# Performance work log

Hardware: AMD Instinct MI355X
Metric: run time of the kernel (lower is better)

## Reference

```python
import jax, jax.numpy as jnp
import numpy as np

N_NODES = 10000
N_EDGES = 640000
F_IN = 128
HID = 128
F_OUT = 40
BN_EPS = 1e-5


def setup_inputs() -> dict:
    key = jax.random.key(0)
    ks = jax.random.split(key, 8)
    x = jax.random.normal(ks[0], (N_NODES, F_IN), dtype=jnp.float32)
    edge_row = jax.random.randint(ks[1], (N_EDGES,), 0, N_NODES)
    edge_col = jax.random.randint(ks[2], (N_EDGES,), 0, N_NODES)
    edge_val = jax.random.uniform(ks[3], (N_EDGES,), dtype=jnp.float32)
    W1 = jax.random.normal(ks[4], (F_IN, HID), dtype=jnp.float32) * 0.05
    W2 = jax.random.normal(ks[5], (HID, HID), dtype=jnp.float32) * 0.05
    W3 = jax.random.normal(ks[6], (HID, F_OUT), dtype=jnp.float32) * 0.05
    return {
        "x": x, "edge_row": edge_row, "edge_col": edge_col, "edge_val": edge_val,
        "W1": W1, "b1": jnp.zeros((HID,), jnp.float32),
        "gamma2": jnp.ones((HID,), jnp.float32), "beta2": jnp.zeros((HID,), jnp.float32),
        "W2": W2, "b2": jnp.zeros((HID,), jnp.float32),
        "gamma3": jnp.ones((HID,), jnp.float32), "beta3": jnp.zeros((HID,), jnp.float32),
        "W3": W3, "b3": jnp.zeros((F_OUT,), jnp.float32),
    }


def _spmm(edge_row, edge_col, edge_val, x, n_nodes):
    # out[i] = sum_{e: row[e]==i} val[e] * x[col[e]]  == torch.sparse.mm(adj, x)
    msgs = edge_val[:, None] * jnp.take(x, edge_col, axis=0)  # [E, F]
    return jax.ops.segment_sum(msgs, edge_row, num_segments=n_nodes)


def _batchnorm(x, gamma, beta):
    # BatchNorm1d (training-mode normalization, biased variance)
    mean = jnp.mean(x, axis=0)
    var = jnp.mean(jnp.square(x - mean), axis=0)
    return gamma * (x - mean) * jax.lax.rsqrt(var + BN_EPS) + beta


def reference(x, edge_row, edge_col, edge_val, W1, b1, gamma2, beta2,
              W2, b2, gamma3, beta3, W3, b3):
    n = x.shape[0]
    # layer 1: SpMM -> Linear -> ReLU -> (dropout=identity in eval) -> BN
    h = _spmm(edge_row, edge_col, edge_val, x, n)
    h = jax.nn.relu(h @ W1 + b1)
    h = _batchnorm(h, gamma2, beta2)
    # layer 2
    h = _spmm(edge_row, edge_col, edge_val, h, n)
    h = jax.nn.relu(h @ W2 + b2)
    h = _batchnorm(h, gamma3, beta3)
    # layer 3
    h = _spmm(edge_row, edge_col, edge_val, h, n)
    h = h @ W3 + b3
    return jax.nn.log_softmax(h, axis=1)
```

## Files before the change

kernel.cpp:

```cpp
#include <hip/hip_runtime.h>
#include <hip/hip_bf16.h>
#include <math.h>

#define N_NODES 10000
#define F 128
#define F_OUT_ 40
#define N_EDGES_ 640000
#define BN_EPS 1e-5f
#define NBIN 625
#define RPB 16
#define NWGA 64
#define EPW 10000
#define BINCAP 1536
#define NREP 8

__device__ __forceinline__ unsigned pack4(int col, float v) {
    __hip_bfloat16 b = __float2bfloat16(v);
    return ((unsigned)(*(unsigned short*)&b) << 16) | (unsigned)col;
}
__device__ __forceinline__ int   col_of(unsigned q) { return (int)(q & 0xFFFFu); }
__device__ __forceinline__ float val_of(unsigned q) { return __uint_as_float(q & 0xFFFF0000u); }
__device__ __forceinline__ float lo16f(unsigned w) { return __uint_as_float(w << 16); }
__device__ __forceinline__ float hi16f(unsigned w) { return __uint_as_float(w & 0xffff0000u); }

__global__ __launch_bounds__(256) void fused_g1h(const float* __restrict__ x,
        const float* __restrict__ W1, __hip_bfloat16* __restrict__ T,
        const int* __restrict__ erow, int* __restrict__ hist,
        float* __restrict__ accsZ ) {
    __shared__ float Ws[F * F];
    __shared__ float As[16][F];
    __shared__ int   lh[NBIN];
    int tid = threadIdx.x;
    if (blockIdx.x == 0) {
        for (int i = tid; i < 2 * NREP * 256; i += 256) accsZ[i] = 0.f;
    }
    if (blockIdx.x >= NBIN) {
        int w = blockIdx.x - NBIN;
        for (int t = tid; t < NBIN; t += 256) lh[t] = 0;
        __syncthreads();
        int e0 = w * EPW;
        for (int e = e0 + tid; e < e0 + EPW; e += 256)
            atomicAdd(&lh[erow[e] >> 4], 1);
        __syncthreads();
        for (int t = tid; t < NBIN; t += 256) hist[w * NBIN + t] = lh[t];
        return;
    }
    for (int i = tid; i < F * F; i += 256) Ws[i] = W1[i];
    int r0 = blockIdx.x * 16;
    for (int i = tid; i < 16 * F; i += 256) {
        int r2 = i >> 7, k = i & (F - 1);
        As[r2][k] = x[(size_t)(r0 + r2) * F + k];
    }
    __syncthreads();
    int c = tid & (F - 1), hh = tid >> 7;
    for (int r2 = hh; r2 < 16; r2 += 2) {
        float acc = 0.f;
        #pragma unroll
        for (int k = 0; k < F; ++k) acc = fmaf(As[r2][k], Ws[k * F + c], acc);
        T[(size_t)(r0 + r2) * F + c] = __float2bfloat16(acc);
    }
}

__global__ __launch_bounds__(1024) void scatter_bin(const int* __restrict__ erow,
                                                    const int* __restrict__ ecol,
                                                    const float* __restrict__ eval_,
                                                    const int* __restrict__ hist,
                                                    int* __restrict__ base_g,
                                                    int2* __restrict__ ebin) {
    __shared__ int myoff[NBIN];
    __shared__ int tot[NBIN];
    __shared__ int cur[NBIN];
    __shared__ int sc[1024];
    int w = blockIdx.x, tid = threadIdx.x;
    for (int b = tid; b < NBIN; b += 1024) {
        int own = 0, all = 0;
        #pragma unroll 8
        for (int w2 = 0; w2 < NWGA; ++w2) {
            int h = hist[w2 * NBIN + b];
            all += h;
            if (w2 < w) own += h;
        }
        myoff[b] = own;
        tot[b] = all;
        cur[b] = 0;
    }
    __syncthreads();
    int val = (tid < NBIN) ? tot[tid] : 0;
    sc[tid] = val;
    __syncthreads();
    for (int off = 1; off < 1024; off <<= 1) {
        int v = 0;
        if (tid >= off) v = sc[tid - off];
        __syncthreads();
        if (tid >= off) sc[tid] += v;
        __syncthreads();
    }
    if (tid < NBIN) {
        int base = sc[tid] - val;
        myoff[tid] += base;
        if (w == 0) base_g[tid] = base;
    }
    if (w == 0 && tid == 0) base_g[NBIN] = N_EDGES_;
    __syncthreads();
    int e0 = w * EPW, e1 = e0 + EPW;
    int e = e0 + tid;
    for (; e + 3072 < e1; e += 4096) {
        int   r0 = erow[e],        r1 = erow[e + 1024],  r2 = erow[e + 2048],  r3 = erow[e + 3072];
        int   c0 = ecol[e],        c1 = ecol[e + 1024],  c2 = ecol[e + 2048],  c3 = ecol[e + 3072];
        float v0 = eval_[e],       v1 = eval_[e + 1024], v2 = eval_[e + 2048], v3 = eval_[e + 3072];
        int b0 = r0 >> 4, b1 = r1 >> 4, b2 = r2 >> 4, b3 = r3 >> 4;
        int p0 = atomicAdd(&cur[b0], 1);
        int p1 = atomicAdd(&cur[b1], 1);
        int p2 = atomicAdd(&cur[b2], 1);
        int p3 = atomicAdd(&cur[b3], 1);
        ebin[myoff[b0] + p0] = make_int2((r0 << 14) | c0, __float_as_int(v0));
        ebin[myoff[b1] + p1] = make_int2((r1 << 14) | c1, __float_as_int(v1));
        ebin[myoff[b2] + p2] = make_int2((r2 << 14) | c2, __float_as_int(v2));
        ebin[myoff[b3] + p3] = make_int2((r3 << 14) | c3, __float_as_int(v3));
    }
    for (; e < e1; e += 1024) {
        int r = erow[e];
        int b = r >> 4;
        int p = atomicAdd(&cur[b], 1);
        ebin[myoff[b] + p] = make_int2((r << 14) | ecol[e], __float_as_int(eval_[e]));
    }
}

__global__ __launch_bounds__(256) void sort_bin(const int* __restrict__ base,
                                                const int2* __restrict__ ebin,
                                                unsigned* __restrict__ ebin2,
                                                int* __restrict__ rowptr) {
    __shared__ int2    ein[BINCAP];
    __shared__ unsigned eout[BINCAP];
    __shared__ int cnt16[16], pos16[16], exc[16];
    int b = blockIdx.x, tid = threadIdx.x;
    int lo = base[b], hi = base[b + 1];
    int n = min(hi - lo, BINCAP);
    for (int i = tid; i < n; i += 256) ein[i] = ebin[lo + i];
    if (tid < 16) cnt16[tid] = 0;
    __syncthreads();
    for (int i = tid; i < n; i += 256)
        atomicAdd(&cnt16[(ein[i].x >> 14) & 15], 1);
    __syncthreads();
    if (tid == 0) {
        int run = 0;
        #pragma unroll
        for (int j = 0; j < 16; ++j) { exc[j] = run; run += cnt16[j]; }
    }
    __syncthreads();
    if (tid < 16) {
        pos16[tid] = exc[tid];
        rowptr[b * RPB + tid] = lo + exc[tid];
    }
    if (b == NBIN - 1 && tid == 0) rowptr[N_NODES] = hi;
    __syncthreads();
    for (int i = tid; i < n; i += 256) {
        int2 q = ein[i];
        int j = (q.x >> 14) & 15;
        int p = atomicAdd(&pos16[j], 1);
        eout[p] = pack4(q.x & 16383, __int_as_float(q.y));
    }
    __syncthreads();
    for (int i = tid; i < n; i += 256) ebin2[lo + i] = eout[i];
}

__global__ __launch_bounds__(256) void spmm_row4s(const int* __restrict__ rowptr,
                                                  const unsigned* __restrict__ epk,
                                                  const uint2* __restrict__ T2,
                                                  float* __restrict__ Z,
                                                  const float* __restrict__ bias,
                                                  float* __restrict__ accs) {
    __shared__ float sacc[2][F];
    int tid = threadIdx.x;
    for (int i = tid; i < 2 * F; i += 256) ((float*)sacc)[i] = 0.f;
    __syncthreads();
    int wv = tid >> 6, lane = tid & 63;
    int r = blockIdx.x * 4 + wv;
    int beg = rowptr[r], end = rowptr[r + 1];
    int half = lane >> 5, l2 = lane & 31;
    float a0c0 = 0.f, a0c1 = 0.f, a1c0 = 0.f, a1c1 = 0.f;
    float a2c0 = 0.f, a2c1 = 0.f, a3c0 = 0.f, a3c1 = 0.f;
    for (int bb = beg; bb < end; bb += 64) {
        int m = min(end - bb, 64);
        unsigned myq = (lane < m) ? epk[bb + lane] : 0u;
        int j = 0;
        for (; j + 16 <= m; j += 16) {
            unsigned q[8]; uint2 w[8];
            #pragma unroll
            for (int t = 0; t < 8; ++t) {
                q[t] = __shfl(myq, j + 2 * t + half);
                w[t] = T2[(unsigned)col_of(q[t]) * 32u + l2];
            }
            #pragma unroll
            for (int t = 0; t < 8; ++t) {
                float v = val_of(q[t]);
                if (t & 1) {
                    a0c1 = fmaf(v, lo16f(w[t].x), a0c1);
                    a1c1 = fmaf(v, hi16f(w[t].x), a1c1);
                    a2c1 = fmaf(v, lo16f(w[t].y), a2c1);
                    a3c1 = fmaf(v, hi16f(w[t].y), a3c1);
                } else {
                    a0c0 = fmaf(v, lo16f(w[t].x), a0c0);
                    a1c0 = fmaf(v, hi16f(w[t].x), a1c0);
                    a2c0 = fmaf(v, lo16f(w[t].y), a2c0);
                    a3c0 = fmaf(v, hi16f(w[t].y), a3c0);
                }
            }
        }
        for (; j + 2 <= m; j += 2) {
            unsigned q = __shfl(myq, j + half);
            uint2 w = T2[(unsigned)col_of(q) * 32u + l2];
            float v = val_of(q);
            a0c0 = fmaf(v, lo16f(w.x), a0c0);
            a1c0 = fmaf(v, hi16f(w.x), a1c0);
            a2c0 = fmaf(v, lo16f(w.y), a2c0);
            a3c0 = fmaf(v, hi16f(w.y), a3c0);
        }
        if (j < m) {
            unsigned q = __shfl(myq, j);
            uint2 w = T2[(unsigned)col_of(q) * 32u + l2];
            float v = half ? 0.f : val_of(q);
            a0c0 = fmaf(v, lo16f(w.x), a0c0);
            a1c0 = fmaf(v, hi16f(w.x), a1c0);
            a2c0 = fmaf(v, lo16f(w.y), a2c0);
            a3c0 = fmaf(v, hi16f(w.y), a3c0);
        }
    }
    float a0 = a0c0 + a0c1, a1 = a1c0 + a1c1;
    float a2 = a2c0 + a2c1, a3 = a3c0 + a3c1;
    a0 += __shfl_xor(a0, 32);
    a1 += __shfl_xor(a1, 32);
    a2 += __shfl_xor(a2, 32);
    a3 += __shfl_xor(a3, 32);
    if (half == 0) {
        *(float4*)(Z + (size_t)r * F + 4 * l2) = make_float4(a0, a1, a2, a3);
        float4 bi = *(const float4*)(bias + 4 * l2);
        float t0 = fmaxf(a0 + bi.x, 0.f), t1 = fmaxf(a1 + bi.y, 0.f);
        float t2 = fmaxf(a2 + bi.z, 0.f), t3 = fmaxf(a3 + bi.w, 0.f);
        atomicAdd(&sacc[0][4 * l2],     t0); atomicAdd(&sacc[1][4 * l2],     t0 * t0);
        atomicAdd(&sacc[0][4 * l2 + 1], t1); atomicAdd(&sacc[1][4 * l2 + 1], t1 * t1);
        atomicAdd(&sacc[0][4 * l2 + 2], t2); atomicAdd(&sacc[1][4 * l2 + 2], t2 * t2);
        atomicAdd(&sacc[0][4 * l2 + 3], t3); atomicAdd(&sacc[1][4 * l2 + 3], t3 * t3);
    }
    __syncthreads();
    int rep = blockIdx.x & (NREP - 1);
    float* dst = accs + rep * 2 * F;
    for (int i = tid; i < F; i += 256) {
        atomicAdd(&dst[i],     sacc[0][i]);
        atomicAdd(&dst[F + i], sacc[1][i]);
    }
}

__global__ __launch_bounds__(256) void spmm40_ls(const int* __restrict__ rowptr,
                                                 const unsigned* __restrict__ epk,
                                                 const unsigned short* __restrict__ T40,
                                                 const float* __restrict__ b3,
                                                 float* __restrict__ out) {
    int wv = threadIdx.x >> 6, lane = threadIdx.x & 63;
    int w = blockIdx.x * 4 + wv;
    if (w >= N_NODES) return;
    int beg = rowptr[w], end = rowptr[w + 1];
    float a[4] = {0.f, 0.f, 0.f, 0.f};
    const unsigned short* Tb = T40 + lane;
    bool act = (lane < F_OUT_);
    for (int base = beg; base < end; base += 64) {
        int m = min(end - base, 64);
        unsigned myq = 0;
        if (lane < m) myq = epk[base + lane];
        int j = 0;
        for (; j + 8 <= m; j += 8) {
            unsigned q[8];
            #pragma unroll
            for (int t = 0; t < 8; ++t) q[t] = __shfl(myq, j + t);
            if (act) {
                unsigned short u[8];
                #pragma unroll
                for (int t = 0; t < 8; ++t) u[t] = Tb[(unsigned)col_of(q[t]) * 40u];
                #pragma unroll
                for (int t = 0; t < 8; ++t)
                    a[t & 3] = fmaf(val_of(q[t]),
                                    __uint_as_float(((unsigned)u[t]) << 16), a[t & 3]);
            }
        }
        for (; j < m; ++j) {
            unsigned q = __shfl(myq, j);
            if (act) {
                unsigned short u = Tb[(unsigned)col_of(q) * 40u];
                a[0] = fmaf(val_of(q), __uint_as_float(((unsigned)u) << 16), a[0]);
            }
        }
    }
    float acc = (a[0] + a[1]) + (a[2] + a[3]);
    float val = act ? acc + b3[lane] : -INFINITY;
    float m2 = val;
    #pragma unroll
    for (int off = 32; off > 0; off >>= 1) m2 = fmaxf(m2, __shfl_xor(m2, off));
    float e = act ? expf(val - m2) : 0.f;
    float s = e;
    #pragma unroll
    for (int off = 32; off > 0; off >>= 1) s += __shfl_xor(s, off);
    if (act) out[(size_t)w * F_OUT_ + lane] = val - m2 - logf(s);
}


__global__ __launch_bounds__(256) void gemm128_bn(const float* __restrict__ A,
        const float* __restrict__ W, const float* __restrict__ bias,
        const float* __restrict__ gamma, const float* __restrict__ beta,
        const float* __restrict__ accs, __hip_bfloat16* __restrict__ C) {
    __shared__ float Ws[F * F];
    __shared__ float As[16][F];
    __shared__ float sc[F], sh[F], bi[F];
    int tid = threadIdx.x;
    if (tid < F) {
        float s = 0.f, s2 = 0.f;
        #pragma unroll
        for (int rp = 0; rp < NREP; ++rp) {
            s  += accs[rp * 2 * F + tid];
            s2 += accs[rp * 2 * F + F + tid];
        }
        float m   = s / (float)N_NODES;
        float var = s2 / (float)N_NODES - m * m;
        float rs  = rsqrtf(var + BN_EPS);
        float g   = gamma[tid] * rs;
        sc[tid] = g;
        sh[tid] = beta[tid] - g * m;
        bi[tid] = bias[tid];
    }
    for (int i = tid; i < F * F; i += 256) Ws[i] = W[i];
    __syncthreads();
    int r0 = blockIdx.x * 16;
    for (int i = tid; i < 16 * F; i += 256) {
        int r2 = i >> 7, k = i & (F - 1);
        float a = A[(size_t)(r0 + r2) * F + k];
        As[r2][k] = fmaxf(a + bi[k], 0.f) * sc[k] + sh[k];
    }
    __syncthreads();
    int c = tid & (F - 1), hh = tid >> 7;
    for (int r2 = hh; r2 < 16; r2 += 2) {
        float acc = 0.f;
        #pragma unroll
        for (int k = 0; k < F; ++k) acc = fmaf(As[r2][k], Ws[k * F + c], acc);
        C[(size_t)(r0 + r2) * F + c] = __float2bfloat16(acc);
    }
}

__global__ __launch_bounds__(256) void gemm40_bn(const float* __restrict__ A,
        const float* __restrict__ W, const float* __restrict__ bias,
        const float* __restrict__ gamma, const float* __restrict__ beta,
        const float* __restrict__ accs, __hip_bfloat16* __restrict__ C) {
    __shared__ float Ws[F * F_OUT_];
    __shared__ float sc[F], sh[F], bi[F];
    int tid = threadIdx.x;
    if (tid < F) {
        float s = 0.f, s2 = 0.f;
        #pragma unroll
        for (int rp = 0; rp < NREP; ++rp) {
            s  += accs[rp * 2 * F + tid];
            s2 += accs[rp * 2 * F + F + tid];
        }
        float m   = s / (float)N_NODES;
        float var = s2 / (float)N_NODES - m * m;
        float rs  = rsqrtf(var + BN_EPS);
        float g   = gamma[tid] * rs;
        sc[tid] = g;
        sh[tid] = beta[tid] - g * m;
        bi[tid] = bias[tid];
    }
    for (int i = tid; i < F * F_OUT_; i += 256) Ws[i] = W[i];
    __syncthreads();
    int c = tid % F_OUT_, rl = tid / F_OUT_;
    if (rl >= 6) return;
    int r = blockIdx.x * 6 + rl;
    if (r >= N_NODES) return;
    const float* a = A + (size_t)r * F;
    float acc = 0.f;
    #pragma unroll
    for (int k = 0; k < F; ++k) {
        float t = fmaxf(a[k] + bi[k], 0.f) * sc[k] + sh[k];
        acc = fmaf(t, Ws[k * F_OUT_ + c], acc);
    }
    C[(size_t)r * F_OUT_ + c] = __float2bfloat16(acc);
}


extern "C" void kernel_launch(void* const* d_in, const int* in_sizes, int n_in,
                              void* d_out, int out_size, void* d_ws, size_t ws_size,
                              hipStream_t stream) {
    const float* x      = (const float*)d_in[0];
    const int*   erow   = (const int*)  d_in[1];
    const int*   ecol   = (const int*)  d_in[2];
    const float* eval_  = (const float*)d_in[3];
    const float* W1     = (const float*)d_in[4];
    const float* b1     = (const float*)d_in[5];
    const float* gamma2 = (const float*)d_in[6];
    const float* beta2  = (const float*)d_in[7];
    const float* W2     = (const float*)d_in[8];
    const float* b2     = (const float*)d_in[9];
    const float* gamma3 = (const float*)d_in[10];
    const float* beta3  = (const float*)d_in[11];
    const float* W3     = (const float*)d_in[12];
    const float* b3     = (const float*)d_in[13];
    float* out = (float*)d_out;

    const size_t nf = (size_t)N_NODES * F;
    const int BLK = 256;

    int*   hist   = (int*)d_ws;
    int*   base_g = hist + NWGA * NBIN;
    float* accsA  = (float*)(base_g + 626);
    float* accsB  = accsA + NREP * 256;
    int*   rowptr = (int*)(accsB + NREP * 256);
    __hip_bfloat16* T = (__hip_bfloat16*)(rowptr + 10016);
    float* Z     = (float*)((char*)T + nf * 2);
    int2*  ebin  = (int2*)(Z + nf);
    unsigned* ebin2 = (unsigned*)(ebin + N_EDGES_);

    fused_g1h<<<NBIN + NWGA, BLK, 0, stream>>>(x, W1, T, erow, hist, accsA);
    scatter_bin<<<NWGA, 1024, 0, stream>>>(erow, ecol, eval_, hist, base_g, ebin);
    sort_bin<<<NBIN, BLK, 0, stream>>>(base_g, ebin, ebin2, rowptr);

    const int GB4 = N_NODES / 4;

    spmm_row4s<<<GB4, BLK, 0, stream>>>(rowptr, ebin2, (const uint2*)T, Z, b1, accsA);

    gemm128_bn<<<NBIN, BLK, 0, stream>>>(Z, W2, b1, gamma2, beta2, accsA, T);
    spmm_row4s<<<GB4, BLK, 0, stream>>>(rowptr, ebin2, (const uint2*)T, Z, b2, accsB);

    gemm40_bn<<<(N_NODES + 5) / 6, BLK, 0, stream>>>(Z, W3, b2, gamma3, beta3, accsB, T);
    spmm40_ls<<<GB4, BLK, 0, stream>>>(rowptr, ebin2, (const unsigned short*)T, b3, out);
}
```

Baseline: 149.9 us.

## Use nontemporal gathers in SpMM and spread edge scatter over more workgroups

The SpMM kernels now read the gathered feature table through nontemporal loads, which changes how the random gathers interact with the caches. The edge-binning pass now uses 256 workgroups of 2500 edges each instead of 64 of 10000, and its 4-way unrolled loop is replaced by a simple strided loop. The nontemporal hint may hurt reuse, because T is small and rows are gathered many times. The larger histogram also makes the prefix work in the binning kernels bigger.

```diff
diff --git a/kernel.cpp b/kernel.cpp
--- a/kernel.cpp
+++ b/kernel.cpp
@@ -9,8 +9,8 @@
 #define BN_EPS 1e-5f
 #define NBIN 625
 #define RPB 16
-#define NWGA 64
-#define EPW 10000
+#define NWGA 256
+#define EPW 2500
 #define BINCAP 1536
 #define NREP 8
 
@@ -103,22 +103,7 @@
     if (w == 0 && tid == 0) base_g[NBIN] = N_EDGES_;
     __syncthreads();
     int e0 = w * EPW, e1 = e0 + EPW;
-    int e = e0 + tid;
-    for (; e + 3072 < e1; e += 4096) {
-        int   r0 = erow[e],        r1 = erow[e + 1024],  r2 = erow[e + 2048],  r3 = erow[e + 3072];
-        int   c0 = ecol[e],        c1 = ecol[e + 1024],  c2 = ecol[e + 2048],  c3 = ecol[e + 3072];
-        float v0 = eval_[e],       v1 = eval_[e + 1024], v2 = eval_[e + 2048], v3 = eval_[e + 3072];
-        int b0 = r0 >> 4, b1 = r1 >> 4, b2 = r2 >> 4, b3 = r3 >> 4;
-        int p0 = atomicAdd(&cur[b0], 1);
-        int p1 = atomicAdd(&cur[b1], 1);
-        int p2 = atomicAdd(&cur[b2], 1);
-        int p3 = atomicAdd(&cur[b3], 1);
-        ebin[myoff[b0] + p0] = make_int2((r0 << 14) | c0, __float_as_int(v0));
-        ebin[myoff[b1] + p1] = make_int2((r1 << 14) | c1, __float_as_int(v1));
-        ebin[myoff[b2] + p2] = make_int2((r2 << 14) | c2, __float_as_int(v2));
-        ebin[myoff[b3] + p3] = make_int2((r3 << 14) | c3, __float_as_int(v3));
-    }
-    for (; e < e1; e += 1024) {
+    for (int e = e0 + tid; e < e1; e += 1024) {
         int r = erow[e];
         int b = r >> 4;
         int p = atomicAdd(&cur[b], 1);
@@ -166,7 +151,7 @@
 
 __global__ __launch_bounds__(256) void spmm_row4s(const int* __restrict__ rowptr,
                                                   const unsigned* __restrict__ epk,
-                                                  const uint2* __restrict__ T2,
+                                                  const unsigned long long* __restrict__ T8,
                                                   float* __restrict__ Z,
                                                   const float* __restrict__ bias,
                                                   float* __restrict__ accs) {
@@ -185,45 +170,48 @@
         unsigned myq = (lane < m) ? epk[bb + lane] : 0u;
         int j = 0;
         for (; j + 16 <= m; j += 16) {
-            unsigned q[8]; uint2 w[8];
+            unsigned q[8]; unsigned long long w[8];
             #pragma unroll
             for (int t = 0; t < 8; ++t) {
                 q[t] = __shfl(myq, j + 2 * t + half);
-                w[t] = T2[(unsigned)col_of(q[t]) * 32u + l2];
+                w[t] = __builtin_nontemporal_load(T8 + (unsigned)col_of(q[t]) * 32u + l2);
             }
             #pragma unroll
             for (int t = 0; t < 8; ++t) {
                 float v = val_of(q[t]);
+                unsigned wx = (unsigned)w[t], wy = (unsigned)(w[t] >> 32);
                 if (t & 1) {
-                    a0c1 = fmaf(v, lo16f(w[t].x), a0c1);
-                    a1c1 = fmaf(v, hi16f(w[t].x), a1c1);
-                    a2c1 = fmaf(v, lo16f(w[t].y), a2c1);
-                    a3c1 = fmaf(v, hi16f(w[t].y), a3c1);
+                    a0c1 = fmaf(v, lo16f(wx), a0c1);
+                    a1c1 = fmaf(v, hi16f(wx), a1c1);
+                    a2c1 = fmaf(v, lo16f(wy), a2c1);
+                    a3c1 = fmaf(v, hi16f(wy), a3c1);
                 } else {
-                    a0c0 = fmaf(v, lo16f(w[t].x), a0c0);
-                    a1c0 = fmaf(v, hi16f(w[t].x), a1c0);
-                    a2c0 = fmaf(v, lo16f(w[t].y), a2c0);
-                    a3c0 = fmaf(v, hi16f(w[t].y), a3c0);
+                    a0c0 = fmaf(v, lo16f(wx), a0c0);
+                    a1c0 = fmaf(v, hi16f(wx), a1c0);
+                    a2c0 = fmaf(v, lo16f(wy), a2c0);
+                    a3c0 = fmaf(v, hi16f(wy), a3c0);
                 }
             }
         }
         for (; j + 2 <= m; j += 2) {
             unsigned q = __shfl(myq, j + half);
-            uint2 w = T2[(unsigned)col_of(q) * 32u + l2];
+            unsigned long long w = __builtin_nontemporal_load(T8 + (unsigned)col_of(q) * 32u + l2);
             float v = val_of(q);
-            a0c0 = fmaf(v, lo16f(w.x), a0c0);
-            a1c0 = fmaf(v, hi16f(w.x), a1c0);
-            a2c0 = fmaf(v, lo16f(w.y), a2c0);
-            a3c0 = fmaf(v, hi16f(w.y), a3c0);
+            unsigned wx = (unsigned)w, wy = (unsigned)(w >> 32);
+            a0c0 = fmaf(v, lo16f(wx), a0c0);
+            a1c0 = fmaf(v, hi16f(wx), a1c0);
+            a2c0 = fmaf(v, lo16f(wy), a2c0);
+            a3c0 = fmaf(v, hi16f(wy), a3c0);
         }
         if (j < m) {
             unsigned q = __shfl(myq, j);
-            uint2 w = T2[(unsigned)col_of(q) * 32u + l2];
+            unsigned long long w = __builtin_nontemporal_load(T8 + (unsigned)col_of(q) * 32u + l2);
             float v = half ? 0.f : val_of(q);
-            a0c0 = fmaf(v, lo16f(w.x), a0c0);
-            a1c0 = fmaf(v, hi16f(w.x), a1c0);
-            a2c0 = fmaf(v, lo16f(w.y), a2c0);
-            a3c0 = fmaf(v, hi16f(w.y), a3c0);
+            unsigned wx = (unsigned)w, wy = (unsigned)(w >> 32);
+            a0c0 = fmaf(v, lo16f(wx), a0c0);
+            a1c0 = fmaf(v, hi16f(wx), a1c0);
+            a2c0 = fmaf(v, lo16f(wy), a2c0);
+            a3c0 = fmaf(v, hi16f(wy), a3c0);
         }
     }
     float a0 = a0c0 + a0c1, a1 = a1c0 + a1c1;
@@ -275,7 +263,8 @@
             if (act) {
                 unsigned short u[8];
                 #pragma unroll
-                for (int t = 0; t < 8; ++t) u[t] = Tb[(unsigned)col_of(q[t]) * 40u];
+                for (int t = 0; t < 8; ++t)
+                    u[t] = __builtin_nontemporal_load(Tb + (unsigned)col_of(q[t]) * 40u);
                 #pragma unroll
                 for (int t = 0; t < 8; ++t)
                     a[t & 3] = fmaf(val_of(q[t]),
@@ -285,7 +274,7 @@
         for (; j < m; ++j) {
             unsigned q = __shfl(myq, j);
             if (act) {
-                unsigned short u = Tb[(unsigned)col_of(q) * 40u];
+                unsigned short u = __builtin_nontemporal_load(Tb + (unsigned)col_of(q) * 40u);
                 a[0] = fmaf(val_of(q), __uint_as_float(((unsigned)u) << 16), a[0]);
             }
         }
@@ -421,10 +410,10 @@
 
     const int GB4 = N_NODES / 4;
 
-    spmm_row4s<<<GB4, BLK, 0, stream>>>(rowptr, ebin2, (const uint2*)T, Z, b1, accsA);
+    spmm_row4s<<<GB4, BLK, 0, stream>>>(rowptr, ebin2, (const unsigned long long*)T, Z, b1, accsA);
 
     gemm128_bn<<<NBIN, BLK, 0, stream>>>(Z, W2, b1, gamma2, beta2, accsA, T);
-    spmm_row4s<<<GB4, BLK, 0, stream>>>(rowptr, ebin2, (const uint2*)T, Z, b2, accsB);
+    spmm_row4s<<<GB4, BLK, 0, stream>>>(rowptr, ebin2, (const unsigned long long*)T, Z, b2, accsB);
 
     gemm40_bn<<<(N_NODES + 5) / 6, BLK, 0, stream>>>(Z, W3, b2, gamma3, beta3, accsB, T);
     spmm40_ls<<<GB4, BLK, 0, stream>>>(rowptr, ebin2, (const unsigned short*)T, b3, out);
```

Result: slower. 162.8 us (+8.6%).
